# Kernel optimization log

Measured on AMD Instinct MI355X. Metric: run time of the kernel, lower is better.

The kernel has to match this reference:

```python
import jax, jax.numpy as jnp
import numpy as np

V, A, L = 10000, 600, 6          # dx vocab, num ancestors, ancestors-per-leaf
O, E = 128, 128                  # ontoEmbDim, EHREmbDim
ATD, PTD, DPL = 128, 128, 500    # ontoattnDim, ptattnDim, dpLabelSize
B, T, N = 64, 32, 40             # batch, visits, codes-per-visit


def _l2norm(x):
    return x / jnp.maximum(jnp.linalg.norm(x, axis=-1, keepdims=True), 1e-12)


def setup_inputs() -> dict:
    key = jax.random.key(0)
    ks = jax.random.split(key, 16)
    g = lambda k, shape, fan: (jax.random.normal(k, shape) / np.sqrt(fan)).astype(jnp.float32)
    dxseqs = jax.random.randint(ks[0], (B, T, N), 0, V + 1)          # V = padding idx
    dx_onehot = jax.random.uniform(ks[1], (T, B, V), dtype=jnp.float32)
    leaves = jax.random.randint(ks[2], (V, L), 0, V)
    ancestors = jax.random.randint(ks[3], (V, L), V, V + A)
    ehr_table = g(ks[4], (V + 1, E), E).at[V].set(0.0)               # padding row zero
    return dict(
        dxseqs=dxseqs, dx_onehot=dx_onehot, leaves=leaves, ancestors=ancestors,
        onto_table=g(ks[5], (V + A, O), O),
        onto_Wa=g(ks[6], (2 * O, ATD), 2 * O), onto_ba=jnp.zeros((ATD,), jnp.float32),
        onto_Wc=g(ks[7], (ATD, 1), ATD), onto_bc=jnp.zeros((1,), jnp.float32),
        ehr_table=ehr_table,
        attn_W=g(ks[8], (2 * E + 2 * O, PTD), 2 * E + 2 * O), attn_b=jnp.zeros((PTD,), jnp.float32),
        comb_W=g(ks[9], (PTD, 1), PTD), comb_b=jnp.zeros((1,), jnp.float32),
        co_W=g(ks[10], (E, V), E), co_b=jnp.zeros((V,), jnp.float32),
        dp_W=g(ks[11], (O + E, DPL), O + E), dp_b=jnp.zeros((DPL,), jnp.float32),
    )


def _forward(dxseqs, dx_onehot, leaves, ancestors, onto_table, onto_Wa, onto_ba,
             onto_Wc, onto_bc, ehr_table, attn_W, attn_b, comb_W, comb_b,
             co_W, co_b, dp_W, dp_b):
    # --- OntoEmb (GRAM-style ancestor attention) ---
    el = onto_table[leaves]                                  # (V, L, O)
    ea = onto_table[ancestors]                               # (V, L, O)
    h = jnp.tanh(jnp.concatenate([el, ea], -1) @ onto_Wa + onto_ba)
    a = jax.nn.softmax(h @ onto_Wc + onto_bc, axis=1)        # (V, L, 1)
    onto_all = jnp.concatenate(
        [jnp.sum(a * ea, axis=1), jnp.zeros((1, O), onto_table.dtype)], axis=0)  # (V+1, O)

    dxOnto = onto_all[dxseqs]                                # (B, T, N, O)
    ontoV = jnp.einsum('tbv,vo->bto', dx_onehot, onto_all[:-1])  # (B, T, O)
    dxEHR = ehr_table[dxseqs]                                # (B, T, N, E)
    ehrV = _l2norm(jnp.sum(dxEHR, axis=2))                   # (B, T, E)

    # --- cooccurrence branch ---
    cooccurU = jax.nn.softmax(ehrV @ co_W + co_b, axis=2)    # (B, T, V)
    vonehot = jnp.transpose(dx_onehot, (1, 0, 2))            # (B, T, V)
    cooccur_loss = -jnp.mean(jnp.sum(vonehot * jnp.log(cooccurU), axis=(1, 2)))

    # --- additive (Bahdanau) attention over codes in a visit ---
    dxEmb = jnp.concatenate([dxEHR, dxOnto], -1)             # (B, T, N, E+O)
    vs = jnp.concatenate([ontoV, ehrV], -1)[:, :, None, :]   # (B, T, 1, O+E)
    attnInput = jnp.concatenate([jnp.broadcast_to(vs, dxEmb.shape), dxEmb], -1)
    mlp = jnp.tanh(attnInput @ attn_W + attn_b)              # (B, T, N, PTD)
    attn = jax.nn.softmax(mlp @ comb_W + comb_b, axis=2)     # (B, T, N, 1)
    vs2 = jnp.sum(attn * dxEmb, axis=2)                      # (B, T, E+O)

    dp = jax.nn.softmax(jnp.tanh(_l2norm(vs2)) @ dp_W + dp_b, axis=2)  # (B, T, DPL)
    return dp, cooccur_loss * 10.0


def reference(dxseqs, dx_onehot, leaves, ancestors, onto_table, onto_Wa, onto_ba,
              onto_Wc, onto_bc, ehr_table, attn_W, attn_b, comb_W, comb_b,
              co_W, co_b, dp_W, dp_b):
    return _forward(dxseqs, dx_onehot, leaves, ancestors, onto_table, onto_Wa, onto_ba,
                    onto_Wc, onto_bc, ehr_table, attn_W, attn_b, comb_W, comb_b,
                    co_W, co_b, dp_W, dp_b)
```

## Files before the change

kernel.cpp:

```cpp
#include <hip/hip_runtime.h>
#include <math.h>

typedef float4 f4;
typedef __bf16 bf16x8 __attribute__((ext_vector_type(8)));
typedef float f32x4 __attribute__((ext_vector_type(4)));

static constexpr int kV = 10000, kL = 6, kDPL = 500;
static constexpr int kB = 64, kT = 32, kN = 40, kBT = 2048;
static constexpr int kC = 8, kKPER = 1280;
static constexpr int kVT = 79;
static constexpr int kOntoLd = 10240;
static constexpr int kVpad = 10112;

#define MFMA16 __builtin_amdgcn_mfma_f32_16x16x32_bf16

__device__ __forceinline__ bf16x8 cvt8(f4 a, f4 b) {
  bf16x8 r;
  r[0] = (__bf16)a.x; r[1] = (__bf16)a.y; r[2] = (__bf16)a.z; r[3] = (__bf16)a.w;
  r[4] = (__bf16)b.x; r[5] = (__bf16)b.y; r[6] = (__bf16)b.z; r[7] = (__bf16)b.w;
  return r;
}

__global__ __launch_bounds__(256) void mmore_cvt_bf16(
    const float* __restrict__ in, __bf16* __restrict__ out, int n) {
  int i = (blockIdx.x * 256 + threadIdx.x) * 8;
  if (i < n) {
    f4 a = *(const f4*)(in + i), b = *(const f4*)(in + i + 4);
    *(bf16x8*)(out + i) = cvt8(a, b);
  }
}

__global__ __launch_bounds__(256) void mmore_trcvt(
    const float* __restrict__ in, __bf16* __restrict__ out,
    int K, int N, int Kpad) {
  int t = threadIdx.x;
  int n = blockIdx.y * 16 + (t & 15);
  int kb = (blockIdx.x * 16 + (t >> 4)) * 8;
  bf16x8 r;
  #pragma unroll
  for (int i = 0; i < 8; ++i) {
    int k = kb + i;
    float v = (k < K && n < N) ? in[(size_t)k * N + n] : 0.f;
    r[i] = (__bf16)v;
  }
  *(bf16x8*)(out + (size_t)n * Kpad + kb) = r;
}

__global__ __launch_bounds__(128) void mmore_ehrv(
    const int* __restrict__ dxseqs, const float* __restrict__ ehr_table,
    float* __restrict__ ehrV) {
  int bt = blockIdx.x, t = threadIdx.x;
  const int* row = dxseqs + bt * kN;
  float acc = 0.f;
  for (int n = 0; n < kN; ++n) acc += ehr_table[(size_t)row[n] * 128 + t];
  float v = acc * acc;
  #pragma unroll
  for (int off = 32; off; off >>= 1) v += __shfl_down(v, off);
  __shared__ float red[2];
  if ((t & 63) == 0) red[t >> 6] = v;
  __syncthreads();
  float ss = red[0] + red[1];
  float inv = 1.f / fmaxf(sqrtf(ss), 1e-12f);
  ehrV[bt * 128 + t] = acc * inv;
}

__global__ __launch_bounds__(256) void mmore_scores_mfma(
    const __bf16* __restrict__ otb, const int* __restrict__ leaves,
    const int* __restrict__ anc, const __bf16* __restrict__ WaT,
    const float* __restrict__ ba, const float* __restrict__ Wc,
    const float* __restrict__ bc, float* __restrict__ s_out) {
  int t = threadIdx.x, wave = t >> 6, lane = t & 63, lm = lane & 15, lg = lane >> 4;
  int r0 = blockIdx.x * 32;
  int rA0 = r0 + lm, rA1 = rA0 + 16;
  int v0 = rA0 / 6, l0 = rA0 - v0 * 6, v1 = rA1 / 6, l1 = rA1 - v1 * 6;
  const __bf16* pL0 = otb + (size_t)leaves[v0 * 6 + l0] * 128;
  const __bf16* pA0 = otb + (size_t)anc[v0 * 6 + l0] * 128;
  const __bf16* pL1 = otb + (size_t)leaves[v1 * 6 + l1] * 128;
  const __bf16* pA1 = otb + (size_t)anc[v1 * 6 + l1] * 128;
  const __bf16* bp = WaT + (size_t)(wave * 32 + lm) * 256 + lg * 8;
  f32x4 acc[2][2] = {};
  #pragma unroll
  for (int kb = 0; kb < 256; kb += 32) {
    int k = kb + lg * 8;
    const __bf16* s0 = (k < 128) ? (pL0 + k) : (pA0 + (k - 128));
    const __bf16* s1 = (k < 128) ? (pL1 + k) : (pA1 + (k - 128));
    bf16x8 a0 = *(const bf16x8*)s0;
    bf16x8 a1 = *(const bf16x8*)s1;
    bf16x8 b0 = *(const bf16x8*)(bp + kb);
    bf16x8 b1 = *(const bf16x8*)(bp + kb + 16 * 256);
    acc[0][0] = MFMA16(a0, b0, acc[0][0], 0, 0, 0);
    acc[0][1] = MFMA16(a0, b1, acc[0][1], 0, 0, 0);
    acc[1][0] = MFMA16(a1, b0, acc[1][0], 0, 0, 0);
    acc[1][1] = MFMA16(a1, b1, acc[1][1], 0, 0, 0);
  }
  __shared__ float red[4][32];
  float bcv = bc[0];
  #pragma unroll
  for (int mf = 0; mf < 2; ++mf) {
    #pragma unroll
    for (int j = 0; j < 4; ++j) {
      float p = 0.f;
      #pragma unroll
      for (int nf = 0; nf < 2; ++nf) {
        int c = wave * 32 + nf * 16 + lm;
        p += tanhf(acc[mf][nf][j] + ba[c]) * Wc[c];
      }
      #pragma unroll
      for (int off = 8; off; off >>= 1) p += __shfl_xor(p, off);
      if (lm == 0) red[wave][mf * 16 + lg * 4 + j] = p;
    }
  }
  __syncthreads();
  if (t < 32) s_out[r0 + t] = red[0][t] + red[1][t] + red[2][t] + red[3][t] + bcv;
}

__global__ __launch_bounds__(128) void mmore_onto(
    const float* __restrict__ ot, const int* __restrict__ anc,
    const float* __restrict__ s_in, float* __restrict__ onto_all) {
  int v = blockIdx.x, t = threadIdx.x;
  if (v == kV) { onto_all[(size_t)v * 128 + t] = 0.f; return; }
  __shared__ float sv[kL];
  __shared__ int aidx[kL];
  if (t < kL) { sv[t] = s_in[v * kL + t]; aidx[t] = anc[v * kL + t]; }
  __syncthreads();
  float mx = sv[0];
  #pragma unroll
  for (int l = 1; l < kL; ++l) mx = fmaxf(mx, sv[l]);
  float e[kL], sum = 0.f;
  #pragma unroll
  for (int l = 0; l < kL; ++l) { e[l] = expf(sv[l] - mx); sum += e[l]; }
  float acc = 0.f;
  #pragma unroll
  for (int l = 0; l < kL; ++l)
    acc += (e[l] / sum) * ot[(size_t)aidx[l] * 128 + t];
  onto_all[(size_t)v * 128 + t] = acc;
}

__global__ __launch_bounds__(256) void mmore_ontov_mfma(
    const float* __restrict__ X, const __bf16* __restrict__ BT,
    float* __restrict__ part) {
  int t = threadIdx.x, wave = t >> 6, lane = t & 63, lm = lane & 15, lg = lane >> 4;
  int btile = blockIdx.x & 63, chunk = blockIdx.x >> 6;
  int r0 = btile * 32, vbase = chunk * kKPER;
  int Klim = kV - vbase; if (Klim > kKPER) Klim = kKPER;
  int bt0 = r0 + lm, bt1 = bt0 + 16;
  const float* a0 = X + ((size_t)(bt0 & 31) * kB + (bt0 >> 5)) * kV + vbase + lg * 8;
  const float* a1 = X + ((size_t)(bt1 & 31) * kB + (bt1 >> 5)) * kV + vbase + lg * 8;
  const __bf16* bp = BT + (size_t)(wave * 32 + lm) * kOntoLd + vbase + lg * 8;
  f32x4 acc[2][2] = {};
  for (int kb = 0; kb < Klim; kb += 32) {
    bool ka = (vbase + kb + lg * 8) < kV;
    f4 x0 = make_float4(0, 0, 0, 0), x1 = x0, y0 = x0, y1 = x0;
    if (ka) {
      x0 = *(const f4*)(a0 + kb); x1 = *(const f4*)(a0 + kb + 4);
      y0 = *(const f4*)(a1 + kb); y1 = *(const f4*)(a1 + kb + 4);
    }
    bf16x8 af0 = cvt8(x0, x1), af1 = cvt8(y0, y1);
    bf16x8 b0 = *(const bf16x8*)(bp + kb);
    bf16x8 b1 = *(const bf16x8*)(bp + kb + 16 * kOntoLd);
    acc[0][0] = MFMA16(af0, b0, acc[0][0], 0, 0, 0);
    acc[0][1] = MFMA16(af0, b1, acc[0][1], 0, 0, 0);
    acc[1][0] = MFMA16(af1, b0, acc[1][0], 0, 0, 0);
    acc[1][1] = MFMA16(af1, b1, acc[1][1], 0, 0, 0);
  }
  #pragma unroll
  for (int mf = 0; mf < 2; ++mf)
    #pragma unroll
    for (int nf = 0; nf < 2; ++nf) {
      int col = wave * 32 + nf * 16 + lm;
      #pragma unroll
      for (int j = 0; j < 4; ++j) {
        int row = r0 + mf * 16 + lg * 4 + j;
        part[((size_t)chunk * kBT + row) * 128 + col] = acc[mf][nf][j];
      }
    }
}

__global__ __launch_bounds__(256) void mmore_creduce(
    const float* __restrict__ part, float* __restrict__ out) {
  int i = blockIdx.x * 256 + threadIdx.x;
  const int S = kBT * 128;
  float a = 0.f;
  #pragma unroll
  for (int c = 0; c < kC; ++c) a += part[(size_t)c * S + i];
  out[i] = a;
}

__global__ __launch_bounds__(256) void mmore_loss_mfma(
    const float* __restrict__ ehrV, const __bf16* __restrict__ coWT,
    const float* __restrict__ cob, const float* __restrict__ X,
    float* __restrict__ epart) {
  int t = threadIdx.x, wave = t >> 6, lane = t & 63, lm = lane & 15, lg = lane >> 4;
  int vtile = blockIdx.x, btile = blockIdx.y;
  int r0 = btile * 32, vb = vtile * 128;
  const float* a0 = ehrV + (size_t)(r0 + lm) * 128 + lg * 8;
  const float* a1 = a0 + 16 * 128;
  const __bf16* bp = coWT + (size_t)(vb + wave * 32 + lm) * 128 + lg * 8;
  f32x4 acc[2][2] = {};
  #pragma unroll
  for (int kb = 0; kb < 128; kb += 32) {
    f4 x0 = *(const f4*)(a0 + kb), x1 = *(const f4*)(a0 + kb + 4);
    f4 y0 = *(const f4*)(a1 + kb), y1 = *(const f4*)(a1 + kb + 4);
    bf16x8 af0 = cvt8(x0, x1), af1 = cvt8(y0, y1);
    bf16x8 b0 = *(const bf16x8*)(bp + kb);
    bf16x8 b1 = *(const bf16x8*)(bp + kb + 16 * 128);
    acc[0][0] = MFMA16(af0, b0, acc[0][0], 0, 0, 0);
    acc[0][1] = MFMA16(af0, b1, acc[0][1], 0, 0, 0);
    acc[1][0] = MFMA16(af1, b0, acc[1][0], 0, 0, 0);
    acc[1][1] = MFMA16(af1, b1, acc[1][1], 0, 0, 0);
  }
  float se[2][4] = {}, spz[2][4] = {}, sp[2][4] = {};
  #pragma unroll
  for (int nf = 0; nf < 2; ++nf) {
    int c = vb + wave * 32 + nf * 16 + lm;
    if (c < kV) {
      float cb = cob[c];
      #pragma unroll
      for (int mf = 0; mf < 2; ++mf) {
        #pragma unroll
        for (int j = 0; j < 4; ++j) {
          int row = r0 + mf * 16 + lg * 4 + j;
          float z = acc[mf][nf][j] + cb;
          float p = X[((size_t)(row & 31) * kB + (row >> 5)) * kV + c];
          se[mf][j] += __expf(z);
          spz[mf][j] += p * z;
          sp[mf][j] += p;
        }
      }
    }
  }
  __shared__ float red[4][32][3];
  #pragma unroll
  for (int mf = 0; mf < 2; ++mf)
    #pragma unroll
    for (int j = 0; j < 4; ++j) {
      float a = se[mf][j], b = spz[mf][j], d = sp[mf][j];
      #pragma unroll
      for (int off = 8; off; off >>= 1) {
        a += __shfl_xor(a, off); b += __shfl_xor(b, off); d += __shfl_xor(d, off);
      }
      if (lm == 0) {
        int r = mf * 16 + lg * 4 + j;
        red[wave][r][0] = a; red[wave][r][1] = b; red[wave][r][2] = d;
      }
    }
  __syncthreads();
  if (t < 96) {
    int r = t / 3, q = t - (t / 3) * 3;
    float s = red[0][r][q] + red[1][r][q] + red[2][r][q] + red[3][r][q];
    epart[((size_t)vtile * kBT + r0 + r) * 3 + q] = s;
  }
}

__global__ __launch_bounds__(256) void mmore_ereduce(
    const float* __restrict__ epart, float* __restrict__ term) {
  int bt = blockIdx.x * 256 + threadIdx.x;
  float S = 0.f, PZ = 0.f, PS = 0.f;
  for (int c = 0; c < kVT; ++c) {
    size_t o = ((size_t)c * kBT + bt) * 3;
    S += epart[o]; PZ += epart[o + 1]; PS += epart[o + 2];
  }
  term[bt] = PZ - PS * logf(S);
}

__global__ __launch_bounds__(256) void mmore_lossfin(
    const float* __restrict__ term, float* __restrict__ out) {
  int t = threadIdx.x;
  float a = 0.f;
  for (int i = t; i < kBT; i += 256) a += term[i];
  #pragma unroll
  for (int off = 32; off; off >>= 1) a += __shfl_down(a, off);
  __shared__ float red[4];
  if ((t & 63) == 0) red[t >> 6] = a;
  __syncthreads();
  if (t == 0) out[0] = -(10.f / 64.f) * (red[0] + red[1] + red[2] + red[3]);
}

__global__ __launch_bounds__(256) void mmore_gemm_mfma(
    const float* __restrict__ A, const __bf16* __restrict__ WT,
    int ldWT, int koff, const float* __restrict__ bias,
    float* __restrict__ C, int M, int accumulate) {
  int t = threadIdx.x, wave = t >> 6, lane = t & 63, lm = lane & 15, lg = lane >> 4;
  int r0 = blockIdx.x * 32;
  int row0 = r0 + lm, row1 = row0 + 16;
  bool ok0 = row0 < M, ok1 = row1 < M;
  const float* a0 = A + (size_t)row0 * 128 + lg * 8;
  const float* a1 = A + (size_t)row1 * 128 + lg * 8;
  const __bf16* bp = WT + (size_t)(wave * 32 + lm) * ldWT + koff + lg * 8;
  int ld16 = 16 * ldWT;
  f32x4 acc[2][2] = {};
  #pragma unroll
  for (int kb = 0; kb < 128; kb += 32) {
    f4 x0 = make_float4(0, 0, 0, 0), x1 = x0, y0 = x0, y1 = x0;
    if (ok0) { x0 = *(const f4*)(a0 + kb); x1 = *(const f4*)(a0 + kb + 4); }
    if (ok1) { y0 = *(const f4*)(a1 + kb); y1 = *(const f4*)(a1 + kb + 4); }
    bf16x8 af0 = cvt8(x0, x1), af1 = cvt8(y0, y1);
    bf16x8 b0 = *(const bf16x8*)(bp + kb);
    bf16x8 b1 = *(const bf16x8*)(bp + kb + ld16);
    acc[0][0] = MFMA16(af0, b0, acc[0][0], 0, 0, 0);
    acc[0][1] = MFMA16(af0, b1, acc[0][1], 0, 0, 0);
    acc[1][0] = MFMA16(af1, b0, acc[1][0], 0, 0, 0);
    acc[1][1] = MFMA16(af1, b1, acc[1][1], 0, 0, 0);
  }
  #pragma unroll
  for (int mf = 0; mf < 2; ++mf)
    #pragma unroll
    for (int nf = 0; nf < 2; ++nf) {
      int col = wave * 32 + nf * 16 + lm;
      #pragma unroll
      for (int j = 0; j < 4; ++j) {
        int row = r0 + mf * 16 + lg * 4 + j;
        if (row < M) {
          float v = acc[mf][nf][j];
          if (bias) v += bias[col];
          if (accumulate) v += C[(size_t)row * 128 + col];
          C[(size_t)row * 128 + col] = v;
        }
      }
    }
}

__device__ __forceinline__ float mmore_block_sum(float v, float* red) {
  int t = threadIdx.x;
  #pragma unroll
  for (int off = 32; off; off >>= 1) v += __shfl_down(v, off);
  if ((t & 63) == 0) red[t >> 6] = v;
  __syncthreads();
  if (t == 0) red[0] = red[0] + red[1] + red[2] + red[3];
  __syncthreads();
  return red[0];
}

__global__ __launch_bounds__(256) void mmore_attn(
    const int* __restrict__ dxseqs, const float* __restrict__ base,
    const float* __restrict__ pe, const float* __restrict__ po,
    const float* __restrict__ combW, const float* __restrict__ combB,
    const float* __restrict__ ehr_table, const float* __restrict__ onto_all,
    float* __restrict__ tn) {
  __shared__ float base_s[128];
  __shared__ int idx_s[kN];
  __shared__ float scp[kN][2];
  __shared__ float attn_s[64];
  __shared__ float red[4];
  int bt = blockIdx.x, t = threadIdx.x;
  if (t < 128) base_s[t] = base[bt * 128 + t];
  if (t < kN) idx_s[t] = dxseqs[bt * kN + t];
  __syncthreads();
  int c = t & 127, half = t >> 7, wid = t >> 6, lane = t & 63;
  float cw = combW[c];
  for (int n2 = 0; n2 < kN / 2; ++n2) {
    int n = n2 * 2 + half;
    int id = idx_s[n];
    float x = base_s[c] + pe[(size_t)id * 128 + c] + po[(size_t)id * 128 + c];
    float val = tanhf(x) * cw;
    #pragma unroll
    for (int off = 32; off; off >>= 1) val += __shfl_down(val, off);
    if (lane == 0) scp[n][wid & 1] = val;
  }
  __syncthreads();
  if (t < 64) {
    float s = (t < kN) ? (scp[t][0] + scp[t][1] + combB[0]) : -1e30f;
    float mx = s;
    #pragma unroll
    for (int off = 32; off; off >>= 1) mx = fmaxf(mx, __shfl_xor(mx, off));
    float e = (t < kN) ? __expf(s - mx) : 0.f;
    float sm = e;
    #pragma unroll
    for (int off = 32; off; off >>= 1) sm += __shfl_xor(sm, off);
    attn_s[t] = e / sm;
  }
  __syncthreads();
  float acc = 0.f;
  {
    const float* tab = (t < 128) ? ehr_table : onto_all;
    int j = t & 127;
    for (int n = 0; n < kN; ++n)
      acc += attn_s[n] * tab[(size_t)idx_s[n] * 128 + j];
  }
  float ss = mmore_block_sum(acc * acc, red);
  float inv = 1.f / fmaxf(sqrtf(ss), 1e-12f);
  tn[(size_t)bt * 256 + t] = tanhf(acc * inv);
}

__global__ __launch_bounds__(256) void mmore_dpgemm(
    const float* __restrict__ tn, const __bf16* __restrict__ dpWT,
    const float* __restrict__ dpB, float* __restrict__ u) {
  int t = threadIdx.x, wave = t >> 6, lane = t & 63, lm = lane & 15, lg = lane >> 4;
  int c0 = blockIdx.x * 128, r0 = blockIdx.y * 32;
  const float* a0 = tn + (size_t)(r0 + lm) * 256 + lg * 8;
  const float* a1 = a0 + 16 * 256;
  const __bf16* bp = dpWT + (size_t)(c0 + wave * 32 + lm) * 256 + lg * 8;
  f32x4 acc[2][2] = {};
  #pragma unroll
  for (int kb = 0; kb < 256; kb += 32) {
    f4 x0 = *(const f4*)(a0 + kb), x1 = *(const f4*)(a0 + kb + 4);
    f4 y0 = *(const f4*)(a1 + kb), y1 = *(const f4*)(a1 + kb + 4);
    bf16x8 af0 = cvt8(x0, x1), af1 = cvt8(y0, y1);
    bf16x8 b0 = *(const bf16x8*)(bp + kb);
    bf16x8 b1 = *(const bf16x8*)(bp + kb + 16 * 256);
    acc[0][0] = MFMA16(af0, b0, acc[0][0], 0, 0, 0);
    acc[0][1] = MFMA16(af0, b1, acc[0][1], 0, 0, 0);
    acc[1][0] = MFMA16(af1, b0, acc[1][0], 0, 0, 0);
    acc[1][1] = MFMA16(af1, b1, acc[1][1], 0, 0, 0);
  }
  #pragma unroll
  for (int mf = 0; mf < 2; ++mf)
    #pragma unroll
    for (int nf = 0; nf < 2; ++nf) {
      int col = c0 + wave * 32 + nf * 16 + lm;
      float bias = (col < kDPL) ? dpB[col] : 0.f;
      #pragma unroll
      for (int j = 0; j < 4; ++j) {
        int row = r0 + mf * 16 + lg * 4 + j;
        u[(size_t)row * 512 + col] = acc[mf][nf][j] + bias;
      }
    }
}

__global__ __launch_bounds__(128) void mmore_dpsoft(
    const float* __restrict__ u, float* __restrict__ out) {
  int bt = blockIdx.x, t = threadIdx.x;
  __shared__ float red[2];
  float v[4]; float mx = -1e30f;
  #pragma unroll
  for (int i = 0; i < 4; ++i) {
    int c = t + i * 128;
    v[i] = (c < kDPL) ? u[(size_t)bt * 512 + c] : -1e30f;
    mx = fmaxf(mx, v[i]);
  }
  #pragma unroll
  for (int off = 32; off; off >>= 1) mx = fmaxf(mx, __shfl_xor(mx, off));
  if ((t & 63) == 0) red[t >> 6] = mx;
  __syncthreads();
  mx = fmaxf(red[0], red[1]);
  __syncthreads();
  float e[4], s = 0.f;
  #pragma unroll
  for (int i = 0; i < 4; ++i) {
    int c = t + i * 128;
    e[i] = (c < kDPL) ? __expf(v[i] - mx) : 0.f;
    s += e[i];
  }
  #pragma unroll
  for (int off = 32; off; off >>= 1) s += __shfl_xor(s, off);
  if ((t & 63) == 0) red[t >> 6] = s;
  __syncthreads();
  float invS = 1.f / (red[0] + red[1]);
  #pragma unroll
  for (int i = 0; i < 4; ++i) {
    int c = t + i * 128;
    if (c < kDPL) out[(size_t)bt * kDPL + c] = e[i] * invS;
  }
}

extern "C" void kernel_launch(void* const* d_in, const int* in_sizes, int n_in,
                              void* d_out, int out_size, void* d_ws, size_t ws_size,
                              hipStream_t stream) {
  const int*   dxseqs     = (const int*)d_in[0];
  const float* dx_onehot  = (const float*)d_in[1];
  const int*   leaves     = (const int*)d_in[2];
  const int*   ancestors  = (const int*)d_in[3];
  const float* onto_table = (const float*)d_in[4];
  const float* onto_Wa    = (const float*)d_in[5];
  const float* onto_ba    = (const float*)d_in[6];
  const float* onto_Wc    = (const float*)d_in[7];
  const float* onto_bc    = (const float*)d_in[8];
  const float* ehr_table  = (const float*)d_in[9];
  const float* attn_W     = (const float*)d_in[10];
  const float* attn_b     = (const float*)d_in[11];
  const float* comb_W     = (const float*)d_in[12];
  const float* comb_b     = (const float*)d_in[13];
  const float* co_W       = (const float*)d_in[14];
  const float* co_b       = (const float*)d_in[15];
  const float* dp_W       = (const float*)d_in[16];
  const float* dp_b       = (const float*)d_in[17];
  float* out = (float*)d_out;

  float* ws = (float*)d_ws;
  size_t off = 0;
  auto alloc = [&](size_t n) { float* p = ws + off; off += n; return p; };
  float* onto_all = alloc((size_t)(kV + 1) * 128);
  float* s_sc     = alloc((size_t)kV * kL);
  float* ehrV     = alloc((size_t)kBT * 128);
  float* ontoV    = alloc((size_t)kBT * 128);
  float* peR      = alloc((size_t)(kV + 1) * 128);
  float* poR      = alloc((size_t)(kV + 1) * 128);
  float* basep    = alloc((size_t)kBT * 128);
  float* epart    = alloc((size_t)kVT * kBT * 3);
  float* term     = alloc(kBT);
  __bf16* ontoT   = (__bf16*)alloc((size_t)128 * kOntoLd / 2);
  __bf16* coWT    = (__bf16*)alloc((size_t)kVpad * 128 / 2);
  __bf16* attn_WT = (__bf16*)alloc((size_t)128 * 512 / 2);
  __bf16* dpWT    = (__bf16*)alloc((size_t)512 * 256 / 2);
  __bf16* WaT     = (__bf16*)alloc((size_t)128 * 256 / 2);
  __bf16* ot_bf = (__bf16*)peR;
  float*  cpart = peR;
  float*  u     = peR;
  float*  tn    = ehrV;

  mmore_cvt_bf16<<<663, 256, 0, stream>>>(onto_table, ot_bf, 10600 * 128);
  mmore_trcvt<<<dim3(2, 8), 256, 0, stream>>>(onto_Wa, WaT, 256, 128, 256);
  mmore_trcvt<<<dim3(1, 632), 256, 0, stream>>>(co_W, coWT, 128, kV, 128);
  mmore_trcvt<<<dim3(4, 8), 256, 0, stream>>>(attn_W, attn_WT, 512, 128, 512);
  mmore_trcvt<<<dim3(2, 32), 256, 0, stream>>>(dp_W, dpWT, 256, kDPL, 256);

  mmore_ehrv<<<kBT, 128, 0, stream>>>(dxseqs, ehr_table, ehrV);
  mmore_scores_mfma<<<(kV * kL) / 32, 256, 0, stream>>>(
      ot_bf, leaves, ancestors, WaT, onto_ba, onto_Wc, onto_bc, s_sc);
  mmore_onto<<<kV + 1, 128, 0, stream>>>(onto_table, ancestors, s_sc, onto_all);
  mmore_trcvt<<<dim3(80, 8), 256, 0, stream>>>(onto_all, ontoT, kV, 128, kOntoLd);
  mmore_ontov_mfma<<<64 * kC, 256, 0, stream>>>(dx_onehot, ontoT, cpart);
  mmore_creduce<<<(kBT * 128) / 256, 256, 0, stream>>>(cpart, ontoV);
  mmore_loss_mfma<<<dim3(kVT, 64), 256, 0, stream>>>(ehrV, coWT, co_b, dx_onehot, epart);
  mmore_ereduce<<<kBT / 256, 256, 0, stream>>>(epart, term);
  mmore_lossfin<<<1, 256, 0, stream>>>(term, out + (size_t)kBT * kDPL);
  mmore_gemm_mfma<<<313, 256, 0, stream>>>(ehr_table, attn_WT, 512, 256, nullptr, peR, kV + 1, 0);
  mmore_gemm_mfma<<<313, 256, 0, stream>>>(onto_all, attn_WT, 512, 384, nullptr, poR, kV + 1, 0);
  mmore_gemm_mfma<<<64, 256, 0, stream>>>(ontoV, attn_WT, 512, 0, nullptr, basep, kBT, 0);
  mmore_gemm_mfma<<<64, 256, 0, stream>>>(ehrV, attn_WT, 512, 128, attn_b, basep, kBT, 1);
  mmore_attn<<<kBT, 256, 0, stream>>>(dxseqs, basep, peR, poR, comb_W, comb_b,
                                      ehr_table, onto_all, tn);
  mmore_dpgemm<<<dim3(4, 64), 256, 0, stream>>>(tn, dpWT, dp_b, u);
  mmore_dpsoft<<<kBT, 128, 0, stream>>>(u, out);
}
```

Before: 291.7 us.

## Retile ontoV MFMA GEMM with LDS-staged coalesced one-hot loads and more K-chunks

The ontoV GEMM kernel now uses 16-row tiles and 768-wide K chunks, with 13 chunks instead of 8. This more than triples the block count. The dense dx_onehot rows are loaded as coalesced float4 stripes, staged through shared memory, and prefetched one step ahead, so the bandwidth-bound read of the large one-hot tensor streams better and fills more CUs. The larger partial-sum buffer would overlap the transposed co_W copy, so the workspace layout is reordered and the co_W transpose is moved after the reduction. The cost is more partial-sum traffic in the reduce step, extra block barriers, and twice as many B-operand reads per output row.

```diff
diff --git a/kernel.cpp b/kernel.cpp
--- a/kernel.cpp
+++ b/kernel.cpp
@@ -7,7 +7,7 @@
 
 static constexpr int kV = 10000, kL = 6, kDPL = 500;
 static constexpr int kB = 64, kT = 32, kN = 40, kBT = 2048;
-static constexpr int kC = 8, kKPER = 1280;
+static constexpr int kC = 13;
 static constexpr int kVT = 79;
 static constexpr int kOntoLd = 10240;
 static constexpr int kVpad = 10112;
@@ -139,41 +139,65 @@
 __global__ __launch_bounds__(256) void mmore_ontov_mfma(
     const float* __restrict__ X, const __bf16* __restrict__ BT,
     float* __restrict__ part) {
+  __shared__ __align__(16) float a_s[16][68];
   int t = threadIdx.x, wave = t >> 6, lane = t & 63, lm = lane & 15, lg = lane >> 4;
-  int btile = blockIdx.x & 63, chunk = blockIdx.x >> 6;
-  int r0 = btile * 32, vbase = chunk * kKPER;
-  int Klim = kV - vbase; if (Klim > kKPER) Klim = kKPER;
-  int bt0 = r0 + lm, bt1 = bt0 + 16;
-  const float* a0 = X + ((size_t)(bt0 & 31) * kB + (bt0 >> 5)) * kV + vbase + lg * 8;
-  const float* a1 = X + ((size_t)(bt1 & 31) * kB + (bt1 >> 5)) * kV + vbase + lg * 8;
-  const __bf16* bp = BT + (size_t)(wave * 32 + lm) * kOntoLd + vbase + lg * 8;
-  f32x4 acc[2][2] = {};
-  for (int kb = 0; kb < Klim; kb += 32) {
-    bool ka = (vbase + kb + lg * 8) < kV;
-    f4 x0 = make_float4(0, 0, 0, 0), x1 = x0, y0 = x0, y1 = x0;
-    if (ka) {
-      x0 = *(const f4*)(a0 + kb); x1 = *(const f4*)(a0 + kb + 4);
-      y0 = *(const f4*)(a1 + kb); y1 = *(const f4*)(a1 + kb + 4);
-    }
-    bf16x8 af0 = cvt8(x0, x1), af1 = cvt8(y0, y1);
-    bf16x8 b0 = *(const bf16x8*)(bp + kb);
-    bf16x8 b1 = *(const bf16x8*)(bp + kb + 16 * kOntoLd);
-    acc[0][0] = MFMA16(af0, b0, acc[0][0], 0, 0, 0);
-    acc[0][1] = MFMA16(af0, b1, acc[0][1], 0, 0, 0);
-    acc[1][0] = MFMA16(af1, b0, acc[1][0], 0, 0, 0);
-    acc[1][1] = MFMA16(af1, b1, acc[1][1], 0, 0, 0);
-  }
-  #pragma unroll
-  for (int mf = 0; mf < 2; ++mf)
-    #pragma unroll
-    for (int nf = 0; nf < 2; ++nf) {
-      int col = wave * 32 + nf * 16 + lm;
-      #pragma unroll
-      for (int j = 0; j < 4; ++j) {
-        int row = r0 + mf * 16 + lg * 4 + j;
-        part[((size_t)chunk * kBT + row) * 128 + col] = acc[mf][nf][j];
-      }
-    }
+  int btile = blockIdx.x & 127;
+  int chunk = blockIdx.x >> 7;
+  int r0 = btile * 16, vbase = chunk * 768;
+  int srow = t >> 4, scol = (t & 15) * 4;
+  int sbt = r0 + srow;
+  const float* xrow = X + ((size_t)(sbt & 31) * kB + (sbt >> 5)) * kV + vbase;
+  const __bf16* bp0 = BT + (size_t)(wave * 32 + lm) * kOntoLd + vbase + lg * 8;
+  const __bf16* bp1 = bp0 + (size_t)16 * kOntoLd;
+  f32x4 acc0 = {}, acc1 = {};
+  bool last = (chunk == kC - 1);
+  f4 xv = *(const f4*)(xrow + scol);
+  #pragma unroll
+  for (int s = 0; s < 12; ++s) {
+    __syncthreads();
+    *(f4*)&a_s[srow][scol] = xv;
+    __syncthreads();
+    if (s < 11) {
+      xv = *(const f4*)(xrow + (s + 1) * 64 + scol);
+    } else if (last) {
+      f4 z = make_float4(0.f, 0.f, 0.f, 0.f);
+      xv = (scol < 16) ? *(const f4*)(xrow + 768 + scol) : z;
+    }
+    #pragma unroll
+    for (int h = 0; h < 2; ++h) {
+      int kb = s * 64 + h * 32;
+      f4 x0 = *(const f4*)&a_s[lm][h * 32 + lg * 8];
+      f4 x1 = *(const f4*)&a_s[lm][h * 32 + lg * 8 + 4];
+      bf16x8 af = cvt8(x0, x1);
+      bf16x8 b0 = *(const bf16x8*)(bp0 + kb);
+      bf16x8 b1 = *(const bf16x8*)(bp1 + kb);
+      acc0 = MFMA16(af, b0, acc0, 0, 0, 0);
+      acc1 = MFMA16(af, b1, acc1, 0, 0, 0);
+    }
+  }
+  if (last) {
+    __syncthreads();
+    *(f4*)&a_s[srow][scol] = xv;
+    __syncthreads();
+    #pragma unroll
+    for (int h = 0; h < 2; ++h) {
+      int kb = 768 + h * 32;
+      f4 x0 = *(const f4*)&a_s[lm][h * 32 + lg * 8];
+      f4 x1 = *(const f4*)&a_s[lm][h * 32 + lg * 8 + 4];
+      bf16x8 af = cvt8(x0, x1);
+      bf16x8 b0 = *(const bf16x8*)(bp0 + kb);
+      bf16x8 b1 = *(const bf16x8*)(bp1 + kb);
+      acc0 = MFMA16(af, b0, acc0, 0, 0, 0);
+      acc1 = MFMA16(af, b1, acc1, 0, 0, 0);
+    }
+  }
+  #pragma unroll
+  for (int j = 0; j < 4; ++j) {
+    int row = r0 + lg * 4 + j;
+    int col = wave * 32 + lm;
+    part[((size_t)chunk * kBT + row) * 128 + col] = acc0[j];
+    part[((size_t)chunk * kBT + row) * 128 + col + 16] = acc1[j];
+  }
 }
 
 __global__ __launch_bounds__(256) void mmore_creduce(
@@ -483,16 +507,16 @@
   float* s_sc     = alloc((size_t)kV * kL);
   float* ehrV     = alloc((size_t)kBT * 128);
   float* ontoV    = alloc((size_t)kBT * 128);
+  __bf16* ontoT   = (__bf16*)alloc((size_t)128 * kOntoLd / 2);
+  __bf16* attn_WT = (__bf16*)alloc((size_t)128 * 512 / 2);
+  __bf16* dpWT    = (__bf16*)alloc((size_t)512 * 256 / 2);
+  __bf16* WaT     = (__bf16*)alloc((size_t)128 * 256 / 2);
   float* peR      = alloc((size_t)(kV + 1) * 128);
   float* poR      = alloc((size_t)(kV + 1) * 128);
   float* basep    = alloc((size_t)kBT * 128);
   float* epart    = alloc((size_t)kVT * kBT * 3);
   float* term     = alloc(kBT);
-  __bf16* ontoT   = (__bf16*)alloc((size_t)128 * kOntoLd / 2);
   __bf16* coWT    = (__bf16*)alloc((size_t)kVpad * 128 / 2);
-  __bf16* attn_WT = (__bf16*)alloc((size_t)128 * 512 / 2);
-  __bf16* dpWT    = (__bf16*)alloc((size_t)512 * 256 / 2);
-  __bf16* WaT     = (__bf16*)alloc((size_t)128 * 256 / 2);
   __bf16* ot_bf = (__bf16*)peR;
   float*  cpart = peR;
   float*  u     = peR;
@@ -500,7 +524,6 @@
 
   mmore_cvt_bf16<<<663, 256, 0, stream>>>(onto_table, ot_bf, 10600 * 128);
   mmore_trcvt<<<dim3(2, 8), 256, 0, stream>>>(onto_Wa, WaT, 256, 128, 256);
-  mmore_trcvt<<<dim3(1, 632), 256, 0, stream>>>(co_W, coWT, 128, kV, 128);
   mmore_trcvt<<<dim3(4, 8), 256, 0, stream>>>(attn_W, attn_WT, 512, 128, 512);
   mmore_trcvt<<<dim3(2, 32), 256, 0, stream>>>(dp_W, dpWT, 256, kDPL, 256);
 
@@ -509,8 +532,9 @@
       ot_bf, leaves, ancestors, WaT, onto_ba, onto_Wc, onto_bc, s_sc);
   mmore_onto<<<kV + 1, 128, 0, stream>>>(onto_table, ancestors, s_sc, onto_all);
   mmore_trcvt<<<dim3(80, 8), 256, 0, stream>>>(onto_all, ontoT, kV, 128, kOntoLd);
-  mmore_ontov_mfma<<<64 * kC, 256, 0, stream>>>(dx_onehot, ontoT, cpart);
+  mmore_ontov_mfma<<<128 * kC, 256, 0, stream>>>(dx_onehot, ontoT, cpart);
   mmore_creduce<<<(kBT * 128) / 256, 256, 0, stream>>>(cpart, ontoV);
+  mmore_trcvt<<<dim3(1, 632), 256, 0, stream>>>(co_W, coWT, 128, kV, 128);
   mmore_loss_mfma<<<dim3(kVT, 64), 256, 0, stream>>>(ehrV, coWT, co_b, dx_onehot, epart);
   mmore_ereduce<<<kBT / 256, 256, 0, stream>>>(epart, term);
   mmore_lossfin<<<1, 256, 0, stream>>>(term, out + (size_t)kBT * kDPL);
```

Result: faster. 282.4 us (-3.2%).

## Fuse onehot GEMM with loss-term reductions via augmented B table and LDS prefetch

Applied to the files above, without the earlier changes.

The change rewrites the cooccurrence loss so that sum(p*z) becomes ehrV·(X·coWᵀ) + X·cob and sum(p) becomes X·1. These reductions are folded as extra B rows into the same pass over dx_onehot that computes ontoV, so the large X tensor is read once rather than twice. The X tiles are staged into LDS with global_load_lds, triple-buffered and using a swizzled layout. The loss GEMM now only computes the log-sum-exp over wider 256-column tiles. The trade-offs are a more complex async pipeline with hand-placed waitcnt and barriers, and extra bf16 rounding on the folded terms.

```diff
diff --git a/kernel.cpp b/kernel.cpp
--- a/kernel.cpp
+++ b/kernel.cpp
@@ -7,12 +7,18 @@
 
 static constexpr int kV = 10000, kL = 6, kDPL = 500;
 static constexpr int kB = 64, kT = 32, kN = 40, kBT = 2048;
-static constexpr int kC = 8, kKPER = 1280;
-static constexpr int kVT = 79;
-static constexpr int kOntoLd = 10240;
-static constexpr int kVpad = 10112;
+static constexpr int kXC = 5;
+static constexpr int kNB = 272;
+static constexpr int kLd = 10240;
+static constexpr int kVT2 = 40;
 
 #define MFMA16 __builtin_amdgcn_mfma_f32_16x16x32_bf16
+
+typedef const __attribute__((address_space(1))) unsigned int ga_u32;
+typedef __attribute__((address_space(3))) unsigned int lds_u32;
+__device__ __forceinline__ void gll16(const float* g, float* l) {
+  __builtin_amdgcn_global_load_lds((ga_u32*)g, (lds_u32*)l, 16, 0, 0);
+}
 
 __device__ __forceinline__ bf16x8 cvt8(f4 a, f4 b) {
   bf16x8 r;
@@ -44,6 +50,27 @@
     r[i] = (__bf16)v;
   }
   *(bf16x8*)(out + (size_t)n * Kpad + kb) = r;
+}
+
+__global__ __launch_bounds__(256) void mmore_brow(
+    const float* __restrict__ coW, const float* __restrict__ cob,
+    __bf16* __restrict__ Btab) {
+  int id = blockIdx.x * 256 + threadIdx.x;
+  int rr = id / 1280;
+  int kk = (id - rr * 1280) * 8;
+  bf16x8 r;
+  #pragma unroll
+  for (int i = 0; i < 8; ++i) {
+    int k = kk + i;
+    float v = 0.f;
+    if (k < kV) {
+      if (rr < 128) v = coW[(size_t)rr * kV + k];
+      else if (rr == 128) v = cob[k];
+      else if (rr == 129) v = 1.f;
+    }
+    r[i] = (__bf16)v;
+  }
+  *(bf16x8*)(Btab + (size_t)(128 + rr) * kLd + kk) = r;
 }
 
 __global__ __launch_bounds__(128) void mmore_ehrv(
@@ -136,131 +163,168 @@
   onto_all[(size_t)v * 128 + t] = acc;
 }
 
-__global__ __launch_bounds__(256) void mmore_ontov_mfma(
-    const float* __restrict__ X, const __bf16* __restrict__ BT,
+__global__ __launch_bounds__(512) void mmore_xgemm(
+    const float* __restrict__ X, const __bf16* __restrict__ Btab,
     float* __restrict__ part) {
+  __shared__ __align__(16) float a_s[3][16][32];
+  int t = threadIdx.x, wid = t >> 6, lane = t & 63, lm = lane & 15, lg = lane >> 4;
+  int btile = blockIdx.x & 127, chunk = blockIdx.x >> 7;
+  int r0 = btile * 16, ko = chunk * 2048;
+  int nsteps = (chunk < 4) ? 64 : 56;
+  int srow = (wid << 3) + (lane >> 3);
+  int sg = (lane & 7) ^ (((lane >> 3) & 3) << 1);
+  const float* sptr = X + (size_t)(r0 + srow) * kV + ko + sg * 4;
+  int q1 = (((lg * 2) ^ ((lm & 3) << 1))) << 2;
+  const __bf16* bp0 = Btab + (size_t)(wid * 16 + lm) * kLd + ko + lg * 8;
+  const __bf16* bp1 = bp0 + (size_t)128 * kLd;
+  const __bf16* bp2 = Btab + (size_t)(256 + lm) * kLd + ko + lg * 8;
+  f32x4 acc0 = {}, acc1 = {}, acc2 = {};
+  if (wid < 2) {
+    gll16(sptr, &a_s[0][wid * 8][0]);
+    gll16(sptr + 32, &a_s[1][wid * 8][0]);
+  }
+  for (int s = 0; s < nsteps; ++s) {
+    int cur = s % 3;
+    if (wid < 2) {
+      int s2 = s + 2;
+      if (s2 < nsteps) gll16(sptr + (size_t)s2 * 32, &a_s[s2 % 3][wid * 8][0]);
+      int pend = nsteps - 1 - s;
+      if (pend >= 2)      asm volatile("s_waitcnt vmcnt(2)" ::: "memory");
+      else if (pend == 1) asm volatile("s_waitcnt vmcnt(1)" ::: "memory");
+      else                asm volatile("s_waitcnt vmcnt(0)" ::: "memory");
+    }
+    __builtin_amdgcn_s_barrier();
+    asm volatile("" ::: "memory");
+    f4 x0 = *(const f4*)&a_s[cur][lm][q1];
+    f4 x1 = *(const f4*)&a_s[cur][lm][q1 + 4];
+    bf16x8 af = cvt8(x0, x1);
+    int kb = s * 32;
+    bf16x8 b0 = *(const bf16x8*)(bp0 + kb);
+    bf16x8 b1 = *(const bf16x8*)(bp1 + kb);
+    acc0 = MFMA16(af, b0, acc0, 0, 0, 0);
+    acc1 = MFMA16(af, b1, acc1, 0, 0, 0);
+    if (wid == 0) {
+      bf16x8 b2 = *(const bf16x8*)(bp2 + kb);
+      acc2 = MFMA16(af, b2, acc2, 0, 0, 0);
+    }
+    asm volatile("" ::: "memory");
+    __builtin_amdgcn_s_barrier();
+  }
+  if (chunk == 4) {
+    __syncthreads();
+    if (t < 128) {
+      int r = t >> 3, g = t & 7;
+      int sk = 9984 + ((g ^ ((r & 3) << 1)) << 2);
+      f4 v = make_float4(0.f, 0.f, 0.f, 0.f);
+      if (sk < kV) v = *(const f4*)(X + (size_t)(r0 + r) * kV + sk);
+      *(f4*)&a_s[0][r][g * 4] = v;
+    }
+    __syncthreads();
+    int kb = 56 * 32;
+    f4 x0 = *(const f4*)&a_s[0][lm][q1];
+    f4 x1 = *(const f4*)&a_s[0][lm][q1 + 4];
+    bf16x8 af = cvt8(x0, x1);
+    acc0 = MFMA16(af, *(const bf16x8*)(bp0 + kb), acc0, 0, 0, 0);
+    acc1 = MFMA16(af, *(const bf16x8*)(bp1 + kb), acc1, 0, 0, 0);
+    if (wid == 0) acc2 = MFMA16(af, *(const bf16x8*)(bp2 + kb), acc2, 0, 0, 0);
+  }
+  #pragma unroll
+  for (int j = 0; j < 4; ++j) {
+    int r = r0 + lg * 4 + j;
+    int bt = (r & 63) * kT + (r >> 6);
+    size_t o = ((size_t)chunk * kBT + bt) * kNB;
+    part[o + wid * 16 + lm] = acc0[j];
+    part[o + 128 + wid * 16 + lm] = acc1[j];
+    if (wid == 0) part[o + 256 + lm] = acc2[j];
+  }
+}
+
+__global__ __launch_bounds__(256) void mmore_creduce(
+    const float* __restrict__ part, float* __restrict__ ontoV,
+    float* __restrict__ pwred, float* __restrict__ pc, float* __restrict__ sp) {
+  int bt = blockIdx.x, t = threadIdx.x;
+  for (int c = t; c < kNB; c += 256) {
+    float a = 0.f;
+    #pragma unroll
+    for (int ch = 0; ch < kXC; ++ch)
+      a += part[((size_t)ch * kBT + bt) * kNB + c];
+    if (c < 128) ontoV[(size_t)bt * 128 + c] = a;
+    else if (c < 256) pwred[(size_t)bt * 128 + (c - 128)] = a;
+    else if (c == 256) pc[bt] = a;
+    else if (c == 257) sp[bt] = a;
+  }
+}
+
+__global__ __launch_bounds__(256) void mmore_lossg(
+    const float* __restrict__ ehrV, const __bf16* __restrict__ coWT,
+    const float* __restrict__ cob, float* __restrict__ epart) {
   int t = threadIdx.x, wave = t >> 6, lane = t & 63, lm = lane & 15, lg = lane >> 4;
-  int btile = blockIdx.x & 63, chunk = blockIdx.x >> 6;
-  int r0 = btile * 32, vbase = chunk * kKPER;
-  int Klim = kV - vbase; if (Klim > kKPER) Klim = kKPER;
-  int bt0 = r0 + lm, bt1 = bt0 + 16;
-  const float* a0 = X + ((size_t)(bt0 & 31) * kB + (bt0 >> 5)) * kV + vbase + lg * 8;
-  const float* a1 = X + ((size_t)(bt1 & 31) * kB + (bt1 >> 5)) * kV + vbase + lg * 8;
-  const __bf16* bp = BT + (size_t)(wave * 32 + lm) * kOntoLd + vbase + lg * 8;
-  f32x4 acc[2][2] = {};
-  for (int kb = 0; kb < Klim; kb += 32) {
-    bool ka = (vbase + kb + lg * 8) < kV;
-    f4 x0 = make_float4(0, 0, 0, 0), x1 = x0, y0 = x0, y1 = x0;
-    if (ka) {
-      x0 = *(const f4*)(a0 + kb); x1 = *(const f4*)(a0 + kb + 4);
-      y0 = *(const f4*)(a1 + kb); y1 = *(const f4*)(a1 + kb + 4);
-    }
-    bf16x8 af0 = cvt8(x0, x1), af1 = cvt8(y0, y1);
-    bf16x8 b0 = *(const bf16x8*)(bp + kb);
-    bf16x8 b1 = *(const bf16x8*)(bp + kb + 16 * kOntoLd);
-    acc[0][0] = MFMA16(af0, b0, acc[0][0], 0, 0, 0);
-    acc[0][1] = MFMA16(af0, b1, acc[0][1], 0, 0, 0);
-    acc[1][0] = MFMA16(af1, b0, acc[1][0], 0, 0, 0);
-    acc[1][1] = MFMA16(af1, b1, acc[1][1], 0, 0, 0);
-  }
-  #pragma unroll
-  for (int mf = 0; mf < 2; ++mf)
-    #pragma unroll
-    for (int nf = 0; nf < 2; ++nf) {
-      int col = wave * 32 + nf * 16 + lm;
-      #pragma unroll
-      for (int j = 0; j < 4; ++j) {
-        int row = r0 + mf * 16 + lg * 4 + j;
-        part[((size_t)chunk * kBT + row) * 128 + col] = acc[mf][nf][j];
-      }
-    }
-}
-
-__global__ __launch_bounds__(256) void mmore_creduce(
-    const float* __restrict__ part, float* __restrict__ out) {
-  int i = blockIdx.x * 256 + threadIdx.x;
-  const int S = kBT * 128;
-  float a = 0.f;
-  #pragma unroll
-  for (int c = 0; c < kC; ++c) a += part[(size_t)c * S + i];
-  out[i] = a;
-}
-
-__global__ __launch_bounds__(256) void mmore_loss_mfma(
-    const float* __restrict__ ehrV, const __bf16* __restrict__ coWT,
-    const float* __restrict__ cob, const float* __restrict__ X,
-    float* __restrict__ epart) {
-  int t = threadIdx.x, wave = t >> 6, lane = t & 63, lm = lane & 15, lg = lane >> 4;
-  int vtile = blockIdx.x, btile = blockIdx.y;
-  int r0 = btile * 32, vb = vtile * 128;
+  int vt = blockIdx.x, btile = blockIdx.y;
+  int r0 = btile * 32, vb = vt * 256;
   const float* a0 = ehrV + (size_t)(r0 + lm) * 128 + lg * 8;
   const float* a1 = a0 + 16 * 128;
-  const __bf16* bp = coWT + (size_t)(vb + wave * 32 + lm) * 128 + lg * 8;
-  f32x4 acc[2][2] = {};
+  f32x4 acc[2][4] = {};
   #pragma unroll
   for (int kb = 0; kb < 128; kb += 32) {
     f4 x0 = *(const f4*)(a0 + kb), x1 = *(const f4*)(a0 + kb + 4);
     f4 y0 = *(const f4*)(a1 + kb), y1 = *(const f4*)(a1 + kb + 4);
     bf16x8 af0 = cvt8(x0, x1), af1 = cvt8(y0, y1);
-    bf16x8 b0 = *(const bf16x8*)(bp + kb);
-    bf16x8 b1 = *(const bf16x8*)(bp + kb + 16 * 128);
-    acc[0][0] = MFMA16(af0, b0, acc[0][0], 0, 0, 0);
-    acc[0][1] = MFMA16(af0, b1, acc[0][1], 0, 0, 0);
-    acc[1][0] = MFMA16(af1, b0, acc[1][0], 0, 0, 0);
-    acc[1][1] = MFMA16(af1, b1, acc[1][1], 0, 0, 0);
-  }
-  float se[2][4] = {}, spz[2][4] = {}, sp[2][4] = {};
-  #pragma unroll
-  for (int nf = 0; nf < 2; ++nf) {
-    int c = vb + wave * 32 + nf * 16 + lm;
+    #pragma unroll
+    for (int nf = 0; nf < 4; ++nf) {
+      int c = vb + wave * 64 + nf * 16 + lm;
+      bf16x8 b = *(const bf16x8*)(coWT + (size_t)c * 128 + kb + lg * 8);
+      acc[0][nf] = MFMA16(af0, b, acc[0][nf], 0, 0, 0);
+      acc[1][nf] = MFMA16(af1, b, acc[1][nf], 0, 0, 0);
+    }
+  }
+  float se[2][4] = {};
+  #pragma unroll
+  for (int nf = 0; nf < 4; ++nf) {
+    int c = vb + wave * 64 + nf * 16 + lm;
     if (c < kV) {
       float cb = cob[c];
       #pragma unroll
-      for (int mf = 0; mf < 2; ++mf) {
+      for (int mf = 0; mf < 2; ++mf)
         #pragma unroll
-        for (int j = 0; j < 4; ++j) {
-          int row = r0 + mf * 16 + lg * 4 + j;
-          float z = acc[mf][nf][j] + cb;
-          float p = X[((size_t)(row & 31) * kB + (row >> 5)) * kV + c];
-          se[mf][j] += __expf(z);
-          spz[mf][j] += p * z;
-          sp[mf][j] += p;
-        }
-      }
-    }
-  }
-  __shared__ float red[4][32][3];
+        for (int j = 0; j < 4; ++j)
+          se[mf][j] += __expf(acc[mf][nf][j] + cb);
+    }
+  }
+  __shared__ float red[4][32];
   #pragma unroll
   for (int mf = 0; mf < 2; ++mf)
     #pragma unroll
     for (int j = 0; j < 4; ++j) {
-      float a = se[mf][j], b = spz[mf][j], d = sp[mf][j];
+      float v = se[mf][j];
       #pragma unroll
-      for (int off = 8; off; off >>= 1) {
-        a += __shfl_xor(a, off); b += __shfl_xor(b, off); d += __shfl_xor(d, off);
-      }
-      if (lm == 0) {
-        int r = mf * 16 + lg * 4 + j;
-        red[wave][r][0] = a; red[wave][r][1] = b; red[wave][r][2] = d;
-      }
-    }
-  __syncthreads();
-  if (t < 96) {
-    int r = t / 3, q = t - (t / 3) * 3;
-    float s = red[0][r][q] + red[1][r][q] + red[2][r][q] + red[3][r][q];
-    epart[((size_t)vtile * kBT + r0 + r) * 3 + q] = s;
-  }
-}
-
-__global__ __launch_bounds__(256) void mmore_ereduce(
+      for (int off = 8; off; off >>= 1) v += __shfl_xor(v, off);
+      if (lm == 0) red[wave][mf * 16 + lg * 4 + j] = v;
+    }
+  __syncthreads();
+  if (t < 32)
+    epart[(size_t)vt * kBT + r0 + t] =
+        red[0][t] + red[1][t] + red[2][t] + red[3][t];
+}
+
+__global__ __launch_bounds__(256) void mmore_lossterm(
+    const float* __restrict__ ehrV, const float* __restrict__ pwred,
+    const float* __restrict__ pc, const float* __restrict__ sp,
     const float* __restrict__ epart, float* __restrict__ term) {
-  int bt = blockIdx.x * 256 + threadIdx.x;
-  float S = 0.f, PZ = 0.f, PS = 0.f;
-  for (int c = 0; c < kVT; ++c) {
-    size_t o = ((size_t)c * kBT + bt) * 3;
-    S += epart[o]; PZ += epart[o + 1]; PS += epart[o + 2];
-  }
-  term[bt] = PZ - PS * logf(S);
+  int t = threadIdx.x;
+  int bt = blockIdx.x * 16 + (t >> 4);
+  int sub = t & 15;
+  const f4* e = (const f4*)(ehrV + (size_t)bt * 128 + sub * 8);
+  const f4* w = (const f4*)(pwred + (size_t)bt * 128 + sub * 8);
+  f4 e0 = e[0], e1 = e[1], w0 = w[0], w1 = w[1];
+  float d = e0.x * w0.x + e0.y * w0.y + e0.z * w0.z + e0.w * w0.w +
+            e1.x * w1.x + e1.y * w1.y + e1.z * w1.z + e1.w * w1.w;
+  float S = 0.f;
+  for (int vt = sub; vt < kVT2; vt += 16) S += epart[(size_t)vt * kBT + bt];
+  #pragma unroll
+  for (int off = 8; off; off >>= 1) {
+    d += __shfl_xor(d, off); S += __shfl_xor(S, off);
+  }
+  if (sub == 0) term[bt] = (d + pc[bt]) - sp[bt] * logf(S);
 }
 
 __global__ __launch_bounds__(256) void mmore_lossfin(
@@ -483,24 +547,26 @@
   float* s_sc     = alloc((size_t)kV * kL);
   float* ehrV     = alloc((size_t)kBT * 128);
   float* ontoV    = alloc((size_t)kBT * 128);
+  __bf16* Btab    = (__bf16*)alloc((size_t)kNB * kLd / 2);
+  __bf16* attn_WT = (__bf16*)alloc((size_t)128 * 512 / 2);
+  __bf16* dpWT    = (__bf16*)alloc((size_t)512 * 256 / 2);
+  __bf16* WaT     = (__bf16*)alloc((size_t)128 * 256 / 2);
   float* peR      = alloc((size_t)(kV + 1) * 128);
   float* poR      = alloc((size_t)(kV + 1) * 128);
   float* basep    = alloc((size_t)kBT * 128);
-  float* epart    = alloc((size_t)kVT * kBT * 3);
+  float* epart    = alloc((size_t)kVT2 * kBT);
+  float* pwred    = alloc((size_t)kBT * 128);
+  float* pc       = alloc(kBT);
+  float* sp       = alloc(kBT);
   float* term     = alloc(kBT);
-  __bf16* ontoT   = (__bf16*)alloc((size_t)128 * kOntoLd / 2);
-  __bf16* coWT    = (__bf16*)alloc((size_t)kVpad * 128 / 2);
-  __bf16* attn_WT = (__bf16*)alloc((size_t)128 * 512 / 2);
-  __bf16* dpWT    = (__bf16*)alloc((size_t)512 * 256 / 2);
-  __bf16* WaT     = (__bf16*)alloc((size_t)128 * 256 / 2);
   __bf16* ot_bf = (__bf16*)peR;
   float*  cpart = peR;
+  __bf16* coWT  = (__bf16*)peR;
   float*  u     = peR;
   float*  tn    = ehrV;
 
   mmore_cvt_bf16<<<663, 256, 0, stream>>>(onto_table, ot_bf, 10600 * 128);
   mmore_trcvt<<<dim3(2, 8), 256, 0, stream>>>(onto_Wa, WaT, 256, 128, 256);
-  mmore_trcvt<<<dim3(1, 632), 256, 0, stream>>>(co_W, coWT, 128, kV, 128);
   mmore_trcvt<<<dim3(4, 8), 256, 0, stream>>>(attn_W, attn_WT, 512, 128, 512);
   mmore_trcvt<<<dim3(2, 32), 256, 0, stream>>>(dp_W, dpWT, 256, kDPL, 256);
 
@@ -508,11 +574,13 @@
   mmore_scores_mfma<<<(kV * kL) / 32, 256, 0, stream>>>(
       ot_bf, leaves, ancestors, WaT, onto_ba, onto_Wc, onto_bc, s_sc);
   mmore_onto<<<kV + 1, 128, 0, stream>>>(onto_table, ancestors, s_sc, onto_all);
-  mmore_trcvt<<<dim3(80, 8), 256, 0, stream>>>(onto_all, ontoT, kV, 128, kOntoLd);
-  mmore_ontov_mfma<<<64 * kC, 256, 0, stream>>>(dx_onehot, ontoT, cpart);
-  mmore_creduce<<<(kBT * 128) / 256, 256, 0, stream>>>(cpart, ontoV);
-  mmore_loss_mfma<<<dim3(kVT, 64), 256, 0, stream>>>(ehrV, coWT, co_b, dx_onehot, epart);
-  mmore_ereduce<<<kBT / 256, 256, 0, stream>>>(epart, term);
+  mmore_trcvt<<<dim3(80, 8), 256, 0, stream>>>(onto_all, Btab, kV, 128, kLd);
+  mmore_brow<<<720, 256, 0, stream>>>(co_W, co_b, Btab);
+  mmore_xgemm<<<128 * kXC, 512, 0, stream>>>(dx_onehot, Btab, cpart);
+  mmore_creduce<<<kBT, 256, 0, stream>>>(cpart, ontoV, pwred, pc, sp);
+  mmore_trcvt<<<dim3(1, 640), 256, 0, stream>>>(co_W, coWT, 128, kV, 128);
+  mmore_lossg<<<dim3(kVT2, 64), 256, 0, stream>>>(ehrV, coWT, co_b, epart);
+  mmore_lossterm<<<kBT / 16, 256, 0, stream>>>(ehrV, pwred, pc, sp, epart, term);
   mmore_lossfin<<<1, 256, 0, stream>>>(term, out + (size_t)kBT * kDPL);
   mmore_gemm_mfma<<<313, 256, 0, stream>>>(ehr_table, attn_WT, 512, 256, nullptr, peR, kV + 1, 0);
   mmore_gemm_mfma<<<313, 256, 0, stream>>>(onto_all, attn_WT, 512, 384, nullptr, poR, kV + 1, 0);
```

New measurement: 315.1 us. 8.0% more time.
